# Optimization experiments

Hardware: AMD Instinct MI355X
Metric: run time of the kernel (lower is better)

## Reference

```python
import jax, jax.numpy as jnp
import numpy as np


def setup_inputs() -> dict:
    key = jax.random.key(0)
    ks = jax.random.split(key, 6)
    B = 65536
    x = jax.random.normal(ks[0], (B, 784), dtype=jnp.float32)
    conv_w = jax.random.normal(ks[1], (3, 3), dtype=jnp.float32)
    fc1_w = jax.random.normal(ks[2], (100, 676), dtype=jnp.float32) * (1.0 / np.sqrt(676))
    fc1_b = jax.random.normal(ks[3], (100,), dtype=jnp.float32) * 0.01
    fc2_w = jax.random.normal(ks[4], (10, 100), dtype=jnp.float32) * (1.0 / np.sqrt(100))
    fc2_b = jax.random.normal(ks[5], (10,), dtype=jnp.float32) * 0.01
    return {"x": x, "conv_w": conv_w, "fc1_w": fc1_w, "fc1_b": fc1_b, "fc2_w": fc2_w, "fc2_b": fc2_b}


def reference(x, conv_w, fc1_w, fc1_b, fc2_w, fc2_b):
    B = x.shape[0]
    img = x.reshape(B, 1, 28, 28)  # NCHW, single channel
    kern = conv_w.reshape(1, 1, 3, 3)  # OIHW
    # 'valid' cross-correlation, matching the slicing-based Convolve()
    conv = jax.lax.conv_general_dilated(
        img, kern, window_strides=(1, 1), padding='VALID',
        dimension_numbers=('NCHW', 'OIHW', 'NCHW'))  # [B,1,26,26]
    h = conv.reshape(B, 26 * 26)
    h = jax.nn.relu(h @ fc1_w.T + fc1_b)
    out = h @ fc2_w.T + fc2_b
    return out
```

## Files before the change

### kernel.cpp

```cpp
#include <hip/hip_runtime.h>


typedef short  s16x8 __attribute__((ext_vector_type(8)));
typedef float  f32x4 __attribute__((ext_vector_type(4)));

#define BM   32
#define CSTR 712
#define HSTR 132
#define NT   8
#define KC   22

__device__ __forceinline__ unsigned short f2bf(float f) {
    unsigned int u = __builtin_bit_cast(unsigned int, f);
    u = (u + 0x7fffu + ((u >> 16) & 1u)) >> 16;
    return (unsigned short)u;
}

extern "C" __global__ void __launch_bounds__(256)
prep_w1(const float* __restrict__ W1, const float* __restrict__ b1,
        unsigned short* __restrict__ bw)
{
    int id = blockIdx.x * 256 + threadIdx.x;
    if (id >= NT * KC * 64) return;
    int lane = id & 63;
    int kc   = (id >> 6) % KC;
    int t    = id / (KC * 64);
    int n    = t * 16 + (lane & 15);
    int k0   = kc * 32 + (lane >> 4) * 8;
    unsigned short v[8];
#pragma unroll
    for (int j = 0; j < 8; ++j) {
        int k = k0 + j;
        float f = 0.f;
        if (n < 100) {
            if (k < 676)       f = W1[(size_t)n * 676 + k];
            else if (k == 676) f = b1[n];
        }
        v[j] = f2bf(f);
    }
    *(uint4*)(bw + (size_t)id * 8) = *(const uint4*)v;
}

extern "C" __global__ void __launch_bounds__(256, 4)
digit_model_fused(const float* __restrict__ x,
                  const float* __restrict__ cw9,
                  const unsigned short* __restrict__ bw,
                  const float* __restrict__ W2,
                  const float* __restrict__ b2,
                  float* __restrict__ out)
{
    __shared__ __align__(16) unsigned char smem[BM * CSTR * 2];
    unsigned short* cbuf = (unsigned short*)smem;
    float*          hbuf = (float*)smem;

    const int tid  = threadIdx.x;
    const int lane = tid & 63;
    const int wv   = tid >> 6;
    const int q    = lane >> 4;
    const int mn   = lane & 15;
    const int m0   = blockIdx.x * BM;

    float cw[9];
#pragma unroll
    for (int i = 0; i < 9; ++i) cw[i] = cw9[i];

    for (int p = tid; p < BM * 18; p += 256) {
        int mi = p / 18, qq = p - mi * 18;
        *(unsigned int*)(cbuf + mi * CSTR + 676 + qq * 2) = (qq == 0) ? 0x3F80u : 0u;
    }

    for (int task = tid; task < BM * 26; task += 256) {
        int mi = task / 26, r = task - mi * 26;
        const float* ip = x + (size_t)(m0 + mi) * 784 + r * 28;
        float acc[26];
#pragma unroll
        for (int c = 0; c < 26; ++c) acc[c] = 0.f;
#pragma unroll
        for (int dr = 0; dr < 3; ++dr) {
            float rowv[28];
            const float4* rp = (const float4*)(ip + dr * 28);
#pragma unroll
            for (int g = 0; g < 7; ++g) {
                float4 v = rp[g];
                rowv[g*4+0] = v.x; rowv[g*4+1] = v.y;
                rowv[g*4+2] = v.z; rowv[g*4+3] = v.w;
            }
#pragma unroll
            for (int dc = 0; dc < 3; ++dc) {
                float w = cw[dr*3+dc];
#pragma unroll
                for (int c = 0; c < 26; ++c)
                    acc[c] = fmaf(rowv[c + dc], w, acc[c]);
            }
        }
        unsigned short* dst = cbuf + mi * CSTR + r * 26;
#pragma unroll
        for (int c = 0; c < 26; c += 2)
            *(unsigned int*)(dst + c) =
                (unsigned int)f2bf(acc[c]) | ((unsigned int)f2bf(acc[c+1]) << 16);
    }
    __syncthreads();

    f32x4 acc00, acc01, acc10, acc11;
#pragma unroll
    for (int i = 0; i < 4; ++i) { acc00[i]=0.f; acc01[i]=0.f; acc10[i]=0.f; acc11[i]=0.f; }

    const unsigned short* arow0 = cbuf + mn * CSTR + q * 8;
    const unsigned short* arow1 = cbuf + (16 + mn) * CSTR + q * 8;
    const uint4* bwv = (const uint4*)bw;
    const int t0 = wv, t1 = wv + 4;

    uint4 a0 = *(const uint4*)(arow0);
    uint4 a1 = *(const uint4*)(arow1);
    uint4 b0 = bwv[(t0 * KC) * 64 + lane];
    uint4 b1 = bwv[(t1 * KC) * 64 + lane];
    for (int kc = 0; kc < KC; ++kc) {
        int kn = (kc + 1 < KC) ? kc + 1 : kc;
        uint4 na0 = *(const uint4*)(arow0 + kn * 32);
        uint4 na1 = *(const uint4*)(arow1 + kn * 32);
        uint4 nb0 = bwv[(t0 * KC + kn) * 64 + lane];
        uint4 nb1 = bwv[(t1 * KC + kn) * 64 + lane];
        s16x8 av0 = __builtin_bit_cast(s16x8, a0), av1 = __builtin_bit_cast(s16x8, a1);
        s16x8 bv0 = __builtin_bit_cast(s16x8, b0), bv1 = __builtin_bit_cast(s16x8, b1);
        acc00 = __builtin_amdgcn_mfma_f32_16x16x32_bf16(av0, bv0, acc00, 0, 0, 0);
        acc01 = __builtin_amdgcn_mfma_f32_16x16x32_bf16(av0, bv1, acc01, 0, 0, 0);
        acc10 = __builtin_amdgcn_mfma_f32_16x16x32_bf16(av1, bv0, acc10, 0, 0, 0);
        acc11 = __builtin_amdgcn_mfma_f32_16x16x32_bf16(av1, bv1, acc11, 0, 0, 0);
        a0 = na0; a1 = na1; b0 = nb0; b1 = nb1;
    }
    __syncthreads();

#pragma unroll
    for (int r = 0; r < 4; ++r) {
        int row = q * 4 + r;
        float v;
        v = acc00[r]; v = v > 0.f ? v : 0.f; hbuf[ row       * HSTR + t0 * 16 + mn] = v;
        v = acc01[r]; v = v > 0.f ? v : 0.f; hbuf[ row       * HSTR + t1 * 16 + mn] = v;
        v = acc10[r]; v = v > 0.f ? v : 0.f; hbuf[(row + 16) * HSTR + t0 * 16 + mn] = v;
        v = acc11[r]; v = v > 0.f ? v : 0.f; hbuf[(row + 16) * HSTR + t1 * 16 + mn] = v;
    }
    __syncthreads();

    for (int p = tid; p < BM * 10; p += 256) {
        int mi = p / 10, o = p - mi * 10;
        const float4* hv = (const float4*)(hbuf + mi * HSTR);
        const float4* w2 = (const float4*)(W2 + (size_t)o * 100);
        float s = b2[o];
#pragma unroll
        for (int g = 0; g < 25; ++g) {
            float4 h4 = hv[g], w4 = w2[g];
            s += h4.x*w4.x + h4.y*w4.y + h4.z*w4.z + h4.w*w4.w;
        }
        out[(size_t)(m0 + mi) * 10 + o] = s;
    }
}

extern "C" void kernel_launch(void* const* d_in, const int* in_sizes, int n_in,
                              void* d_out, int out_size, void* d_ws, size_t ws_size,
                              hipStream_t stream) {
    const float* x  = (const float*)d_in[0];
    const float* cw = (const float*)d_in[1];
    const float* W1 = (const float*)d_in[2];
    const float* b1 = (const float*)d_in[3];
    const float* W2 = (const float*)d_in[4];
    const float* b2 = (const float*)d_in[5];
    float* out = (float*)d_out;
    unsigned short* bw = (unsigned short*)d_ws;

    const int B = in_sizes[0] / 784;

    hipLaunchKernelGGL(prep_w1, dim3((NT * KC * 64 + 255) / 256), dim3(256),
                       0, stream, W1, b1, bw);
    hipLaunchKernelGGL(digit_model_fused, dim3(B / BM), dim3(256), 0, stream,
                       x, cw, bw, W2, b2, out);
}
```

Baseline: 332.9 us.

## Fold convolution into fc1 weights and run GEMM directly on raw input

The 3x3 convolution is linear, so the prep kernel now folds it into an effective 100x784 fc1 weight (plus bias column), and the main kernel feeds raw input rows straight into the MFMA GEMM. The per-row conv stencil and its register pressure are gone, and input loads become fully coalesced float4 streams. In exchange the GEMM K dimension grows from 704 to 800, shared memory per block grows, and the occupancy hint drops from 4 to 3 blocks. Input rounding to bf16 now uses a simpler round-half-up.

```diff
diff --git a/kernel.cpp b/kernel.cpp
--- a/kernel.cpp
+++ b/kernel.cpp
@@ -5,20 +5,20 @@
 typedef float  f32x4 __attribute__((ext_vector_type(4)));
 
 #define BM   32
-#define CSTR 712
+#define XP   808
 #define HSTR 132
 #define NT   8
-#define KC   22
+#define KC   25
 
-__device__ __forceinline__ unsigned short f2bf(float f) {
+__device__ __forceinline__ unsigned short f2bf_rtne(float f) {
     unsigned int u = __builtin_bit_cast(unsigned int, f);
     u = (u + 0x7fffu + ((u >> 16) & 1u)) >> 16;
     return (unsigned short)u;
 }
 
 extern "C" __global__ void __launch_bounds__(256)
-prep_w1(const float* __restrict__ W1, const float* __restrict__ b1,
-        unsigned short* __restrict__ bw)
+prep_w1eff(const float* __restrict__ W1, const float* __restrict__ cw9,
+           const float* __restrict__ b1, unsigned short* __restrict__ bw)
 {
     int id = blockIdx.x * 256 + threadIdx.x;
     if (id >= NT * KC * 64) return;
@@ -27,30 +27,44 @@
     int t    = id / (KC * 64);
     int n    = t * 16 + (lane & 15);
     int k0   = kc * 32 + (lane >> 4) * 8;
+
+    float cw[9];
+#pragma unroll
+    for (int i = 0; i < 9; ++i) cw[i] = cw9[i];
+
     unsigned short v[8];
 #pragma unroll
     for (int j = 0; j < 8; ++j) {
         int k = k0 + j;
         float f = 0.f;
         if (n < 100) {
-            if (k < 676)       f = W1[(size_t)n * 676 + k];
-            else if (k == 676) f = b1[n];
+            if (k < 784) {
+                int i = k / 28, jj = k % 28;
+                for (int dr = 0; dr < 3; ++dr)
+                    for (int dc = 0; dc < 3; ++dc) {
+                        int a = i - dr, b = jj - dc;
+                        if (a >= 0 && a < 26 && b >= 0 && b < 26)
+                            f = fmaf(W1[(size_t)n * 676 + a * 26 + b],
+                                     cw[dr * 3 + dc], f);
+                    }
+            } else if (k == 784) {
+                f = b1[n];
+            }
         }
-        v[j] = f2bf(f);
+        v[j] = f2bf_rtne(f);
     }
     *(uint4*)(bw + (size_t)id * 8) = *(const uint4*)v;
 }
 
-extern "C" __global__ void __launch_bounds__(256, 4)
-digit_model_fused(const float* __restrict__ x,
-                  const float* __restrict__ cw9,
-                  const unsigned short* __restrict__ bw,
-                  const float* __restrict__ W2,
-                  const float* __restrict__ b2,
-                  float* __restrict__ out)
+extern "C" __global__ void __launch_bounds__(256, 3)
+digit_gemm(const float* __restrict__ x,
+           const unsigned short* __restrict__ bw,
+           const float* __restrict__ W2,
+           const float* __restrict__ b2,
+           float* __restrict__ out)
 {
-    __shared__ __align__(16) unsigned char smem[BM * CSTR * 2];
-    unsigned short* cbuf = (unsigned short*)smem;
+    __shared__ __align__(16) unsigned char smem[BM * XP * 2];
+    unsigned short* xbuf = (unsigned short*)smem;
     float*          hbuf = (float*)smem;
 
     const int tid  = threadIdx.x;
@@ -60,44 +74,43 @@
     const int mn   = lane & 15;
     const int m0   = blockIdx.x * BM;
 
-    float cw[9];
-#pragma unroll
-    for (int i = 0; i < 9; ++i) cw[i] = cw9[i];
-
-    for (int p = tid; p < BM * 18; p += 256) {
-        int mi = p / 18, qq = p - mi * 18;
-        *(unsigned int*)(cbuf + mi * CSTR + 676 + qq * 2) = (qq == 0) ? 0x3F80u : 0u;
+    {
+        int mi = tid >> 3, u = tid & 7;
+        *(unsigned int*)(xbuf + mi * XP + 784 + u * 2) = (u == 0) ? 0x3F80u : 0u;
     }
 
-    for (int task = tid; task < BM * 26; task += 256) {
-        int mi = task / 26, r = task - mi * 26;
-        const float* ip = x + (size_t)(m0 + mi) * 784 + r * 28;
-        float acc[26];
+    const float4* xg = (const float4*)(x + (size_t)m0 * 784);
+    for (int rr = 0; rr < 3; ++rr) {
+        float4 v[8];
 #pragma unroll
-        for (int c = 0; c < 26; ++c) acc[c] = 0.f;
+        for (int i = 0; i < 8; ++i)
+            v[i] = xg[tid + 256 * (rr * 8 + i)];
 #pragma unroll
-        for (int dr = 0; dr < 3; ++dr) {
-            float rowv[28];
-            const float4* rp = (const float4*)(ip + dr * 28);
-#pragma unroll
-            for (int g = 0; g < 7; ++g) {
-                float4 v = rp[g];
-                rowv[g*4+0] = v.x; rowv[g*4+1] = v.y;
-                rowv[g*4+2] = v.z; rowv[g*4+3] = v.w;
-            }
-#pragma unroll
-            for (int dc = 0; dc < 3; ++dc) {
-                float w = cw[dr*3+dc];
-#pragma unroll
-                for (int c = 0; c < 26; ++c)
-                    acc[c] = fmaf(rowv[c + dc], w, acc[c]);
-            }
+        for (int i = 0; i < 8; ++i) {
+            int g  = tid + 256 * (rr * 8 + i);
+            int mi = g / 196, c4 = g - mi * 196;
+            unsigned int ax = __builtin_bit_cast(unsigned int, v[i].x) + 0x8000u;
+            unsigned int ay = __builtin_bit_cast(unsigned int, v[i].y) + 0x8000u;
+            unsigned int az = __builtin_bit_cast(unsigned int, v[i].z) + 0x8000u;
+            unsigned int aw = __builtin_bit_cast(unsigned int, v[i].w) + 0x8000u;
+            uint2 w;
+            w.x = (ax >> 16) | (ay & 0xffff0000u);
+            w.y = (az >> 16) | (aw & 0xffff0000u);
+            *(uint2*)(xbuf + mi * XP + c4 * 4) = w;
         }
-        unsigned short* dst = cbuf + mi * CSTR + r * 26;
-#pragma unroll
-        for (int c = 0; c < 26; c += 2)
-            *(unsigned int*)(dst + c) =
-                (unsigned int)f2bf(acc[c]) | ((unsigned int)f2bf(acc[c+1]) << 16);
+    }
+    if (tid < 128) {
+        int g  = 6144 + tid;
+        float4 vv = xg[g];
+        int mi = g / 196, c4 = g - mi * 196;
+        unsigned int ax = __builtin_bit_cast(unsigned int, vv.x) + 0x8000u;
+        unsigned int ay = __builtin_bit_cast(unsigned int, vv.y) + 0x8000u;
+        unsigned int az = __builtin_bit_cast(unsigned int, vv.z) + 0x8000u;
+        unsigned int aw = __builtin_bit_cast(unsigned int, vv.w) + 0x8000u;
+        uint2 w;
+        w.x = (ax >> 16) | (ay & 0xffff0000u);
+        w.y = (az >> 16) | (aw & 0xffff0000u);
+        *(uint2*)(xbuf + mi * XP + c4 * 4) = w;
     }
     __syncthreads();
 
@@ -105,8 +118,8 @@
 #pragma unroll
     for (int i = 0; i < 4; ++i) { acc00[i]=0.f; acc01[i]=0.f; acc10[i]=0.f; acc11[i]=0.f; }
 
-    const unsigned short* arow0 = cbuf + mn * CSTR + q * 8;
-    const unsigned short* arow1 = cbuf + (16 + mn) * CSTR + q * 8;
+    const unsigned short* arow0 = xbuf + mn * XP + q * 8;
+    const unsigned short* arow1 = xbuf + (16 + mn) * XP + q * 8;
     const uint4* bwv = (const uint4*)bw;
     const int t0 = wv, t1 = wv + 4;
 
@@ -169,8 +182,8 @@
 
     const int B = in_sizes[0] / 784;
 
-    hipLaunchKernelGGL(prep_w1, dim3((NT * KC * 64 + 255) / 256), dim3(256),
-                       0, stream, W1, b1, bw);
-    hipLaunchKernelGGL(digit_model_fused, dim3(B / BM), dim3(256), 0, stream,
-                       x, cw, bw, W2, b2, out);
+    hipLaunchKernelGGL(prep_w1eff, dim3((NT * KC * 64 + 255) / 256), dim3(256),
+                       0, stream, W1, cw, b1, bw);
+    hipLaunchKernelGGL(digit_gemm, dim3(B / BM), dim3(256), 0, stream,
+                       x, bw, W2, b2, out);
 }
```

Result: faster. 321.7 us (-3.4%).
